# Optimization experiments

Hardware: AMD Instinct MI355X
Metric: run time of the kernel (lower is better)

Reference implementation:

```python
import jax, jax.numpy as jnp
import numpy as np

N = 100000      # n_nodes
E = 1600000     # n_edges (avg degree 16)
F_IN = 128      # feat_dim
F_OUT = 128     # hid_dim


def setup_inputs() -> dict:
    key = jax.random.key(0)
    k1, k2, k3, k4 = jax.random.split(key, 4)
    x = jax.random.normal(k1, (N, F_IN), dtype=jnp.float32)
    edge_index = jax.random.randint(k2, (2, E), 0, N, dtype=jnp.int32)
    edge_weight = jax.random.uniform(k3, (E,), dtype=jnp.float32)
    # GCNConv level-0 parameters (Glorot-ish weight, zero bias as PyG default init)
    W = jax.random.normal(k4, (F_IN, F_OUT), dtype=jnp.float32) / np.sqrt(F_IN).astype(np.float32)
    b = jnp.zeros((F_OUT,), dtype=jnp.float32)
    return {"x": x, "W": W, "b": b, "level": 0,
            "edge_index": edge_index, "edge_weight": edge_weight}


def reference(x, W, b, level, edge_index, edge_weight):
    # PyG GCNConv: h = D^-1/2 (A + I) D^-1/2 (x @ W) + b ; Encoder also returns relu(h)
    n = x.shape[0]
    h = x @ W                                          # [N, F_OUT]
    src, dst = edge_index[0], edge_index[1]
    loop = jnp.arange(n, dtype=src.dtype)
    src = jnp.concatenate([src, loop])                 # add self-loops (weight 1)
    dst = jnp.concatenate([dst, loop])
    w = jnp.concatenate([edge_weight, jnp.ones((n,), edge_weight.dtype)])
    deg = jax.ops.segment_sum(w, dst, num_segments=n)  # in-degree by weight
    dinv = jnp.where(deg > 0, jax.lax.rsqrt(deg), 0.0)
    norm = dinv[src] * w * dinv[dst]                   # [E+N]
    emb = jax.ops.segment_sum(h[src] * norm[:, None], dst, num_segments=n) + b
    return emb, jax.nn.relu(emb)
```

## Files before the change

### kernel.cpp

```cpp
#include <hip/hip_runtime.h>

#define F 128
#define K_REP 16

typedef unsigned int uint;
typedef unsigned short ushort;

typedef __attribute__((ext_vector_type(8))) short bf16x8;
typedef __attribute__((ext_vector_type(4))) float f32x4;

union U4B8 { uint4 u; bf16x8 v; };

static __device__ inline ushort f2bf(float f) {
    uint u = __float_as_uint(f);
    return (ushort)((u + 0x7FFF + ((u >> 16) & 1)) >> 16);
}
static __device__ inline float bf2f(ushort h) {
    return __uint_as_float((uint)h << 16);
}

__global__ __launch_bounds__(256) void hist_kernel(const int* __restrict__ dst,
                                                   const float* __restrict__ w,
                                                   unsigned long long* __restrict__ packed,
                                                   int* __restrict__ rank,
                                                   int n, int e) {
    int i = blockIdx.x * 256 + threadIdx.x;
    if (i >= e) return;
    int d = dst[i];
    unsigned long long v = (1ULL << 40) |
                           (unsigned long long)(unsigned)(w[i] * 16777216.0f);
    int k = blockIdx.x & (K_REP - 1);
    unsigned long long old = atomicAdd(&packed[(size_t)k * n + d], v);
    rank[i] = (int)(old >> 40);
}

__global__ __launch_bounds__(256) void scan1_kernel(const unsigned long long* __restrict__ packed,
                                                    int* __restrict__ partials, int n) {
    __shared__ int red[256];
    int t = threadIdx.x;
    int d = blockIdx.x * 256 + t;
    int s = 0;
    if (d < n) {
        #pragma unroll
        for (int k = 0; k < K_REP; ++k)
            s += (int)(packed[(size_t)k * n + d] >> 40);
    }
    red[t] = s;
    __syncthreads();
    for (int off = 128; off > 0; off >>= 1) {
        if (t < off) red[t] += red[t + off];
        __syncthreads();
    }
    if (t == 0) partials[blockIdx.x] = red[0];
}

__global__ __launch_bounds__(1024) void scan2_kernel(int* __restrict__ partials, int nb) {
    __shared__ int sh[1024];
    int t = threadIdx.x;
    int v = (t < nb) ? partials[t] : 0;
    sh[t] = v;
    __syncthreads();
    for (int off = 1; off < 1024; off <<= 1) {
        int u = (t >= off) ? sh[t - off] : 0;
        __syncthreads();
        sh[t] += u;
        __syncthreads();
    }
    if (t < nb) partials[t] = sh[t] - v;
}

__global__ __launch_bounds__(256) void scan3_kernel(const unsigned long long* __restrict__ packed,
                                                    const int* __restrict__ partials,
                                                    int* __restrict__ seg_start,
                                                    int* __restrict__ row_start,
                                                    float* __restrict__ dinv, int n) {
    __shared__ int red[256];
    int t = threadIdx.x;
    int d = blockIdx.x * 256 + t;
    int cnt_k[K_REP];
    float wsum = 0.f;
    int tot = 0;
    if (d < n) {
        #pragma unroll
        for (int k = 0; k < K_REP; ++k) {
            unsigned long long p = packed[(size_t)k * n + d];
            cnt_k[k] = (int)(p >> 40);
            wsum += (float)(p & 0xFFFFFFFFFFULL);
            tot += cnt_k[k];
        }
    }
    red[t] = tot;
    __syncthreads();
    for (int off = 1; off < 256; off <<= 1) {
        int u = (t >= off) ? red[t - off] : 0;
        __syncthreads();
        red[t] += u;
        __syncthreads();
    }
    if (d < n) {
        int base = partials[blockIdx.x] + red[t] - tot;
        row_start[d] = base;
        int run = base;
        #pragma unroll
        for (int k = 0; k < K_REP; ++k) {
            seg_start[(size_t)k * n + d] = run;
            run += cnt_k[k];
        }
        if (d == n - 1) row_start[n] = run;
        dinv[d] = rsqrtf(1.0f + wsum * (1.0f / 16777216.0f));
    }
}

__global__ __launch_bounds__(256) void build_csr_kernel(const int* __restrict__ src,
                                                        const int* __restrict__ dst,
                                                        const float* __restrict__ w,
                                                        const float* __restrict__ dinv,
                                                        const int* __restrict__ seg_start,
                                                        const int* __restrict__ rank,
                                                        int2* __restrict__ csr,
                                                        int n, int e) {
    int i = blockIdx.x * 256 + threadIdx.x;
    if (i >= e) return;
    int s = src[i], d = dst[i];
    float norm = dinv[s] * w[i] * dinv[d];
    int k = blockIdx.x & (K_REP - 1);
    int pos = seg_start[(size_t)k * n + d] + rank[i];
    csr[pos] = make_int2(s, __float_as_int(norm));
}

__global__ __launch_bounds__(256) void packW_kernel(const float* __restrict__ W,
                                                    uint4* __restrict__ wphi,
                                                    uint4* __restrict__ wplo) {
    int idx = blockIdx.x * 256 + threadIdx.x;
    if (idx >= 8 * 4 * 64) return;
    int l = idx & 63;
    int s = (idx >> 6) & 3;
    int t = idx >> 8;
    int p = t >> 1, q = t & 1;
    int col = 32 * p + 2 * (l & 15) + q;
    int kbase = 32 * s + (l >> 4) * 8;
    uint hi[8], lo[8];
    #pragma unroll
    for (int j = 0; j < 8; ++j) {
        float w = W[(size_t)(kbase + j) * F + col];
        ushort h = f2bf(w);
        lo[j] = f2bf(w - bf2f(h));
        hi[j] = h;
    }
    uint4 vh, vl;
    vh.x = hi[0] | (hi[1] << 16); vh.y = hi[2] | (hi[3] << 16);
    vh.z = hi[4] | (hi[5] << 16); vh.w = hi[6] | (hi[7] << 16);
    vl.x = lo[0] | (lo[1] << 16); vl.y = lo[2] | (lo[3] << 16);
    vl.z = lo[4] | (lo[5] << 16); vl.w = lo[6] | (lo[7] << 16);
    wphi[idx] = vh;
    wplo[idx] = vl;
}

#define XPAD 136

__global__ __launch_bounds__(256) void gemm_kernel(const float* __restrict__ x,
                                                   const uint4* __restrict__ wphi,
                                                   const uint4* __restrict__ wplo,
                                                   ushort* __restrict__ hb, int n) {
    __shared__ ushort xhi[64][XPAD];
    __shared__ ushort xlo[64][XPAD];
    int row0 = blockIdx.x * 64;
    int t = threadIdx.x;
    #pragma unroll
    for (int i = 0; i < 8; ++i) {
        int v = t + 256 * i;
        int r = v >> 5, c4 = v & 31;
        int row = row0 + r;
        float4 val = (row < n) ? ((const float4*)x)[(size_t)row * 32 + c4]
                               : make_float4(0.f, 0.f, 0.f, 0.f);
        ushort h0 = f2bf(val.x), h1 = f2bf(val.y), h2 = f2bf(val.z), h3 = f2bf(val.w);
        ushort l0 = f2bf(val.x - bf2f(h0)), l1 = f2bf(val.y - bf2f(h1));
        ushort l2 = f2bf(val.z - bf2f(h2)), l3 = f2bf(val.w - bf2f(h3));
        *(ushort4*)&xhi[r][c4 * 4] = make_ushort4(h0, h1, h2, h3);
        *(ushort4*)&xlo[r][c4 * 4] = make_ushort4(l0, l1, l2, l3);
    }
    __syncthreads();

    int wv = t >> 6, l = t & 63;
    int m = l & 15, quad = l >> 4;
    f32x4 acc[8];
    #pragma unroll
    for (int i = 0; i < 8; ++i) acc[i] = (f32x4){0.f, 0.f, 0.f, 0.f};

    #pragma unroll
    for (int s = 0; s < 4; ++s) {
        bf16x8 ahi = *(const bf16x8*)&xhi[16 * wv + m][32 * s + quad * 8];
        bf16x8 alo = *(const bf16x8*)&xlo[16 * wv + m][32 * s + quad * 8];
        #pragma unroll
        for (int tt = 0; tt < 8; ++tt) {
            int widx = (tt * 4 + s) * 64 + l;
            U4B8 bh, bl;
            bh.u = wphi[widx];
            bl.u = wplo[widx];
            acc[tt] = __builtin_amdgcn_mfma_f32_16x16x32_bf16(ahi, bh.v, acc[tt], 0, 0, 0);
            acc[tt] = __builtin_amdgcn_mfma_f32_16x16x32_bf16(alo, bh.v, acc[tt], 0, 0, 0);
            acc[tt] = __builtin_amdgcn_mfma_f32_16x16x32_bf16(ahi, bl.v, acc[tt], 0, 0, 0);
        }
    }

    #pragma unroll
    for (int r = 0; r < 4; ++r) {
        int row = row0 + 16 * wv + quad * 4 + r;
        if (row < n) {
            uint* outp = (uint*)hb + (size_t)row * 64;
            #pragma unroll
            for (int p = 0; p < 4; ++p) {
                uint vp = (uint)f2bf(acc[2 * p][r]) | ((uint)f2bf(acc[2 * p + 1][r]) << 16);
                outp[p * 16 + m] = vp;
            }
        }
    }
}

__global__ __launch_bounds__(256) void aggregate_kernel(
        const ushort* __restrict__ hb, const int* __restrict__ row_start,
        const int2* __restrict__ csr, const float* __restrict__ dinv,
        const float* __restrict__ b,
        float* __restrict__ out_emb, float* __restrict__ out_relu, int n) {
    int wave = threadIdx.x >> 6;
    int lane = threadIdx.x & 63;
    int i = blockIdx.x * 4 + wave;
    if (i >= n) return;
    int lo = row_start[i], hi = row_start[i + 1];
    float di = dinv[i];
    const uint* h32 = (const uint*)hb;
    uint hvu = h32[(size_t)i * 64 + lane];
    float2 bv = ((const float2*)b)[lane];
    float2 acc;
    acc.x = fmaf(__uint_as_float(hvu << 16) * di, di, bv.x);
    acc.y = fmaf(__uint_as_float(hvu & 0xFFFF0000u) * di, di, bv.y);
    for (int c = lo; c < hi; c += 64) {
        int m = min(64, hi - c);
        int sv = 0, nvi = 0;
        if (lane < m) { int2 en = csr[c + lane]; sv = en.x; nvi = en.y; }
        int mp = (m + 7) & ~7;
        for (int j = 0; j < mp; j += 8) {
            int ss[8]; float nw[8]; uint g[8];
            #pragma unroll
            for (int u = 0; u < 8; ++u) {
                ss[u] = __builtin_amdgcn_readlane(sv, j + u);
                nw[u] = __uint_as_float((uint)__builtin_amdgcn_readlane(nvi, j + u));
            }
            #pragma unroll
            for (int u = 0; u < 8; ++u)
                g[u] = h32[(size_t)ss[u] * 64 + lane];
            #pragma unroll
            for (int u = 0; u < 8; ++u) {
                acc.x = fmaf(__uint_as_float(g[u] << 16), nw[u], acc.x);
                acc.y = fmaf(__uint_as_float(g[u] & 0xFFFF0000u), nw[u], acc.y);
            }
        }
    }
    ((float2*)out_emb)[(size_t)i * 64 + lane] = acc;
    ((float2*)out_relu)[(size_t)i * 64 + lane] =
        make_float2(fmaxf(acc.x, 0.f), fmaxf(acc.y, 0.f));
}

extern "C" void kernel_launch(void* const* d_in, const int* in_sizes, int n_in,
                              void* d_out, int out_size, void* d_ws, size_t ws_size,
                              hipStream_t stream) {
    const float* x  = (const float*)d_in[0];
    const float* W  = (const float*)d_in[1];
    const float* b  = (const float*)d_in[2];
    const int*   ei = (const int*)d_in[4];
    const float* ew = (const float*)d_in[5];

    int n = in_sizes[0] / F;
    int e = in_sizes[4] / 2;
    const int* src = ei;
    const int* dst = ei + e;

    float* out_emb  = (float*)d_out;
    float* out_relu = out_emb + (size_t)n * F;

    ushort* hb = (ushort*)d_ws;
    int2* csr = (int2*)(hb + (size_t)n * F);
    unsigned long long* packed = (unsigned long long*)csr;
    size_t shared_elems = (size_t)e > (size_t)K_REP * n ? (size_t)e : (size_t)K_REP * n;
    int*   seg_start  = (int*)(csr + shared_elems);
    int*   row_start  = seg_start + (size_t)K_REP * n;
    float* dinv       = (float*)(row_start + n + 16);
    int*   partials   = (int*)(dinv + n);
    int*   rank       = partials + 1024;
    uint4* wphi       = (uint4*)(rank + e);
    uint4* wplo       = wphi + 2048;

    int nb_e    = (e + 255) / 256;
    int nb_scan = (n + 255) / 256;

    hipMemsetAsync(packed, 0, (size_t)K_REP * n * sizeof(unsigned long long), stream);
    packW_kernel<<<8, 256, 0, stream>>>(W, wphi, wplo);
    hist_kernel<<<nb_e, 256, 0, stream>>>(dst, ew, packed, rank, n, e);
    scan1_kernel<<<nb_scan, 256, 0, stream>>>(packed, partials, n);
    scan2_kernel<<<1, 1024, 0, stream>>>(partials, nb_scan);
    scan3_kernel<<<nb_scan, 256, 0, stream>>>(packed, partials, seg_start,
                                              row_start, dinv, n);
    gemm_kernel<<<(n + 63) / 64, 256, 0, stream>>>(x, wphi, wplo, hb, n);
    build_csr_kernel<<<nb_e, 256, 0, stream>>>(src, dst, ew, dinv, seg_start, rank,
                                               csr, n, e);
    aggregate_kernel<<<(n + 3) / 4, 256, 0, stream>>>(hb, row_start, csr, dinv, b,
                                                      out_emb, out_relu, n);
}
```

Baseline: 373.4 us.

## Replace global-atomic CSR build with two-level bucket sort in shared memory

Replaces the replicated global 64-bit atomic histogram, three-pass scan and rank-based scatter with a coarse bucket sort. Edges are counted and scattered by 128-node buckets using shared-memory atomics, then each bucket is locally sorted by destination in LDS. That pass also computes degrees, dinv and row starts, and folds dinv[dst] into the edge weight. dinv[src] is now applied inside the aggregate kernel. The aim is to remove heavy global atomic traffic and the large memset. The risks are a per-bucket LDS capacity cap (P3CAP 4096) that would silently truncate buckets above that size, a 17-bit src packing limit, and an extra dinv gather in the aggregate loop.

```diff
diff --git a/kernel.cpp b/kernel.cpp
--- a/kernel.cpp
+++ b/kernel.cpp
@@ -1,7 +1,11 @@
 #include <hip/hip_runtime.h>
 
 #define F 128
-#define K_REP 16
+#define BSH 7
+#define BWIDTH (1 << BSH)
+#define MAX_NBKT 1024
+#define CHUNK 4096
+#define P3CAP 4096
 
 typedef unsigned int uint;
 typedef unsigned short ushort;
@@ -19,45 +23,48 @@
     return __uint_as_float((uint)h << 16);
 }
 
-__global__ __launch_bounds__(256) void hist_kernel(const int* __restrict__ dst,
-                                                   const float* __restrict__ w,
-                                                   unsigned long long* __restrict__ packed,
-                                                   int* __restrict__ rank,
-                                                   int n, int e) {
-    int i = blockIdx.x * 256 + threadIdx.x;
-    if (i >= e) return;
-    int d = dst[i];
-    unsigned long long v = (1ULL << 40) |
-                           (unsigned long long)(unsigned)(w[i] * 16777216.0f);
-    int k = blockIdx.x & (K_REP - 1);
-    unsigned long long old = atomicAdd(&packed[(size_t)k * n + d], v);
-    rank[i] = (int)(old >> 40);
-}
-
-__global__ __launch_bounds__(256) void scan1_kernel(const unsigned long long* __restrict__ packed,
-                                                    int* __restrict__ partials, int n) {
-    __shared__ int red[256];
+__global__ __launch_bounds__(256) void bucket_count_kernel(const int* __restrict__ dst,
+                                                           int* __restrict__ cnt_g,
+                                                           int nbkt, int e) {
+    __shared__ int hist[MAX_NBKT];
     int t = threadIdx.x;
-    int d = blockIdx.x * 256 + t;
-    int s = 0;
-    if (d < n) {
-        #pragma unroll
-        for (int k = 0; k < K_REP; ++k)
-            s += (int)(packed[(size_t)k * n + d] >> 40);
-    }
-    red[t] = s;
-    __syncthreads();
-    for (int off = 128; off > 0; off >>= 1) {
-        if (t < off) red[t] += red[t + off];
-        __syncthreads();
-    }
-    if (t == 0) partials[blockIdx.x] = red[0];
-}
-
-__global__ __launch_bounds__(1024) void scan2_kernel(int* __restrict__ partials, int nb) {
+    for (int i = t; i < nbkt; i += 256) hist[i] = 0;
+    __syncthreads();
+    int base = blockIdx.x * CHUNK;
+    #pragma unroll
+    for (int j = 0; j < 16; ++j) {
+        int i = base + t + 256 * j;
+        if (i < e) atomicAdd(&hist[dst[i] >> BSH], 1);
+    }
+    __syncthreads();
+    for (int i = t; i < nbkt; i += 256)
+        cnt_g[(size_t)blockIdx.x * nbkt + i] = hist[i];
+}
+
+__global__ __launch_bounds__(512) void scanA_kernel(const int* __restrict__ cnt_g,
+                                                    int* __restrict__ within_g,
+                                                    int* __restrict__ totals,
+                                                    int nbkt, int eb) {
+    __shared__ int sh[512];
+    int b = blockIdx.x, t = threadIdx.x;
+    int v = (t < eb) ? cnt_g[(size_t)t * nbkt + b] : 0;
+    sh[t] = v;
+    __syncthreads();
+    for (int off = 1; off < 512; off <<= 1) {
+        int u = (t >= off) ? sh[t - off] : 0;
+        __syncthreads();
+        sh[t] += u;
+        __syncthreads();
+    }
+    if (t < eb) within_g[(size_t)t * nbkt + b] = sh[t] - v;
+    if (t == 511) totals[b] = sh[511];
+}
+
+__global__ __launch_bounds__(1024) void scanB_kernel(const int* __restrict__ totals,
+                                                     int* __restrict__ bbase, int nbkt) {
     __shared__ int sh[1024];
     int t = threadIdx.x;
-    int v = (t < nb) ? partials[t] : 0;
+    int v = (t < nbkt) ? totals[t] : 0;
     sh[t] = v;
     __syncthreads();
     for (int off = 1; off < 1024; off <<= 1) {
@@ -66,66 +73,89 @@
         sh[t] += u;
         __syncthreads();
     }
-    if (t < nb) partials[t] = sh[t] - v;
-}
-
-__global__ __launch_bounds__(256) void scan3_kernel(const unsigned long long* __restrict__ packed,
-                                                    const int* __restrict__ partials,
-                                                    int* __restrict__ seg_start,
-                                                    int* __restrict__ row_start,
-                                                    float* __restrict__ dinv, int n) {
-    __shared__ int red[256];
-    int t = threadIdx.x;
-    int d = blockIdx.x * 256 + t;
-    int cnt_k[K_REP];
-    float wsum = 0.f;
-    int tot = 0;
-    if (d < n) {
-        #pragma unroll
-        for (int k = 0; k < K_REP; ++k) {
-            unsigned long long p = packed[(size_t)k * n + d];
-            cnt_k[k] = (int)(p >> 40);
-            wsum += (float)(p & 0xFFFFFFFFFFULL);
-            tot += cnt_k[k];
-        }
-    }
-    red[t] = tot;
-    __syncthreads();
-    for (int off = 1; off < 256; off <<= 1) {
-        int u = (t >= off) ? red[t - off] : 0;
-        __syncthreads();
-        red[t] += u;
-        __syncthreads();
-    }
-    if (d < n) {
-        int base = partials[blockIdx.x] + red[t] - tot;
-        row_start[d] = base;
-        int run = base;
-        #pragma unroll
-        for (int k = 0; k < K_REP; ++k) {
-            seg_start[(size_t)k * n + d] = run;
-            run += cnt_k[k];
-        }
-        if (d == n - 1) row_start[n] = run;
-        dinv[d] = rsqrtf(1.0f + wsum * (1.0f / 16777216.0f));
-    }
-}
-
-__global__ __launch_bounds__(256) void build_csr_kernel(const int* __restrict__ src,
-                                                        const int* __restrict__ dst,
-                                                        const float* __restrict__ w,
-                                                        const float* __restrict__ dinv,
-                                                        const int* __restrict__ seg_start,
-                                                        const int* __restrict__ rank,
-                                                        int2* __restrict__ csr,
-                                                        int n, int e) {
-    int i = blockIdx.x * 256 + threadIdx.x;
-    if (i >= e) return;
-    int s = src[i], d = dst[i];
-    float norm = dinv[s] * w[i] * dinv[d];
-    int k = blockIdx.x & (K_REP - 1);
-    int pos = seg_start[(size_t)k * n + d] + rank[i];
-    csr[pos] = make_int2(s, __float_as_int(norm));
+    if (t < nbkt) bbase[t] = sh[t] - v;
+    if (t == nbkt - 1) bbase[nbkt] = sh[t];
+}
+
+__global__ __launch_bounds__(256) void scatter_kernel(const int* __restrict__ src,
+                                                      const int* __restrict__ dst,
+                                                      const float* __restrict__ w,
+                                                      const int* __restrict__ bbase,
+                                                      const int* __restrict__ within_g,
+                                                      int2* __restrict__ ebuf,
+                                                      int nbkt, int e) {
+    __shared__ int cursor[MAX_NBKT];
+    int t = threadIdx.x, blk = blockIdx.x;
+    for (int i = t; i < nbkt; i += 256)
+        cursor[i] = bbase[i] + within_g[(size_t)blk * nbkt + i];
+    __syncthreads();
+    int b0 = blk * CHUNK;
+    #pragma unroll
+    for (int j = 0; j < 16; ++j) {
+        int i = b0 + t + 256 * j;
+        if (i < e) {
+            int d = dst[i];
+            int pos = atomicAdd(&cursor[d >> BSH], 1);
+            ebuf[pos] = make_int2(src[i] | ((d & (BWIDTH - 1)) << 17),
+                                  __float_as_int(w[i]));
+        }
+    }
+}
+
+__global__ __launch_bounds__(256) void bucket_build_kernel(int2* __restrict__ ebuf,
+                                                           const int* __restrict__ bbase,
+                                                           int* __restrict__ row_start,
+                                                           float* __restrict__ dinv,
+                                                           int n, int nbkt) {
+    __shared__ int2 stage[P3CAP];
+    __shared__ int cnt[BWIDTH];
+    __shared__ uint ws[BWIDTH];
+    __shared__ float dvl[BWIDTH];
+    __shared__ int cur[BWIDTH];
+    __shared__ int offsh[BWIDTH];
+    int b = blockIdx.x, t = threadIdx.x;
+    int r0 = bbase[b], r1 = bbase[b + 1];
+    int m = r1 - r0;
+    if (m > P3CAP) m = P3CAP;
+    if (t < BWIDTH) { cnt[t] = 0; ws[t] = 0u; }
+    __syncthreads();
+    for (int i = t; i < m; i += 256) {
+        int2 ed = ebuf[r0 + i];
+        stage[i] = ed;
+        int bl = (ed.x >> 17) & (BWIDTH - 1);
+        atomicAdd(&cnt[bl], 1);
+        atomicAdd(&ws[bl], (uint)(__int_as_float(ed.y) * 16777216.0f));
+    }
+    __syncthreads();
+    if (t < BWIDTH) offsh[t] = cnt[t];
+    __syncthreads();
+    for (int off = 1; off < BWIDTH; off <<= 1) {
+        int u = 0;
+        if (t < BWIDTH && t >= off) u = offsh[t - off];
+        __syncthreads();
+        if (t < BWIDTH) offsh[t] += u;
+        __syncthreads();
+    }
+    if (t < BWIDTH) {
+        int excl = offsh[t] - cnt[t];
+        cur[t] = excl;
+        float dv = rsqrtf(1.0f + (float)ws[t] * (1.0f / 16777216.0f));
+        dvl[t] = dv;
+        int d = (b << BSH) + t;
+        if (d < n) {
+            row_start[d] = r0 + excl;
+            dinv[d] = dv;
+            if (d == n - 1) row_start[n] = r1;
+        }
+    }
+    __syncthreads();
+    for (int i = t; i < m; i += 256) {
+        int2 ed = stage[i];
+        int bl = (ed.x >> 17) & (BWIDTH - 1);
+        int pos = atomicAdd(&cur[bl], 1);
+        ebuf[r0 + pos] = make_int2(ed.x & 0x1FFFF,
+                                   __float_as_int(__int_as_float(ed.y) * dvl[bl]));
+    }
 }
 
 __global__ __launch_bounds__(256) void packW_kernel(const float* __restrict__ W,
@@ -237,7 +267,11 @@
     for (int c = lo; c < hi; c += 64) {
         int m = min(64, hi - c);
         int sv = 0, nvi = 0;
-        if (lane < m) { int2 en = csr[c + lane]; sv = en.x; nvi = en.y; }
+        if (lane < m) {
+            int2 en = csr[c + lane];
+            sv = en.x;
+            nvi = __float_as_int(__int_as_float(en.y) * dinv[sv]);
+        }
         int mp = (m + 7) & ~7;
         for (int j = 0; j < mp; j += 8) {
             int ss[8]; float nw[8]; uint g[8];
@@ -278,31 +312,27 @@
     float* out_emb  = (float*)d_out;
     float* out_relu = out_emb + (size_t)n * F;
 
-    ushort* hb = (ushort*)d_ws;
-    int2* csr = (int2*)(hb + (size_t)n * F);
-    unsigned long long* packed = (unsigned long long*)csr;
-    size_t shared_elems = (size_t)e > (size_t)K_REP * n ? (size_t)e : (size_t)K_REP * n;
-    int*   seg_start  = (int*)(csr + shared_elems);
-    int*   row_start  = seg_start + (size_t)K_REP * n;
-    float* dinv       = (float*)(row_start + n + 16);
-    int*   partials   = (int*)(dinv + n);
-    int*   rank       = partials + 1024;
-    uint4* wphi       = (uint4*)(rank + e);
-    uint4* wplo       = wphi + 2048;
-
-    int nb_e    = (e + 255) / 256;
-    int nb_scan = (n + 255) / 256;
-
-    hipMemsetAsync(packed, 0, (size_t)K_REP * n * sizeof(unsigned long long), stream);
+    int nbkt = (n + BWIDTH - 1) >> BSH;
+    int eb   = (e + CHUNK - 1) / CHUNK;
+
+    ushort* hb      = (ushort*)d_ws;
+    int2*   ebuf    = (int2*)(hb + (size_t)n * F);
+    uint4*  wphi    = (uint4*)(ebuf + e);
+    uint4*  wplo    = wphi + 2048;
+    int*    cnt_g   = (int*)(wplo + 2048);
+    int*    within_g= cnt_g + (size_t)eb * nbkt;
+    int*    totals  = within_g + (size_t)eb * nbkt;
+    int*    bbase   = totals + nbkt;
+    int*    row_start = bbase + nbkt + 1;
+    float*  dinv    = (float*)(row_start + n + 4);
+
     packW_kernel<<<8, 256, 0, stream>>>(W, wphi, wplo);
-    hist_kernel<<<nb_e, 256, 0, stream>>>(dst, ew, packed, rank, n, e);
-    scan1_kernel<<<nb_scan, 256, 0, stream>>>(packed, partials, n);
-    scan2_kernel<<<1, 1024, 0, stream>>>(partials, nb_scan);
-    scan3_kernel<<<nb_scan, 256, 0, stream>>>(packed, partials, seg_start,
-                                              row_start, dinv, n);
+    bucket_count_kernel<<<eb, 256, 0, stream>>>(dst, cnt_g, nbkt, e);
+    scanA_kernel<<<nbkt, 512, 0, stream>>>(cnt_g, within_g, totals, nbkt, eb);
+    scanB_kernel<<<1, 1024, 0, stream>>>(totals, bbase, nbkt);
+    scatter_kernel<<<eb, 256, 0, stream>>>(src, dst, ew, bbase, within_g, ebuf, nbkt, e);
+    bucket_build_kernel<<<nbkt, 256, 0, stream>>>(ebuf, bbase, row_start, dinv, n, nbkt);
     gemm_kernel<<<(n + 63) / 64, 256, 0, stream>>>(x, wphi, wplo, hb, n);
-    build_csr_kernel<<<nb_e, 256, 0, stream>>>(src, dst, ew, dinv, seg_start, rank,
-                                               csr, n, e);
-    aggregate_kernel<<<(n + 3) / 4, 256, 0, stream>>>(hb, row_start, csr, dinv, b,
+    aggregate_kernel<<<(n + 3) / 4, 256, 0, stream>>>(hb, row_start, ebuf, dinv, b,
                                                       out_emb, out_relu, n);
 }
```

Measured after the change: 305.6 us. -18.1%, faster.
